# Performance work log

Hardware: AMD Instinct MI355X
Metric: run time of the kernel (lower is better)

The kernel has to match this reference:

```python
import jax, jax.numpy as jnp
import numpy as np

EPS = 1e-6

def _layer_norm(x, w, b):
    mu = jnp.mean(x, axis=-1, keepdims=True)
    var = jnp.mean((x - mu) ** 2, axis=-1, keepdims=True)
    return (x - mu) * jax.lax.rsqrt(var + EPS) * w + b

def setup_inputs() -> dict:
    key = jax.random.key(0)
    ks = jax.random.split(key, 8)
    B, N, C = 4, 1024, 2048
    H = C * 2  # mlp hidden = 2*feature_dim
    std = 0.01
    x = jax.random.normal(ks[0], (B, N, C), dtype=jnp.float32)
    wq = jax.random.normal(ks[1], (C, C), dtype=jnp.float32) * std
    wk = jax.random.normal(ks[2], (C, C), dtype=jnp.float32) * std
    wv = jax.random.normal(ks[3], (C, C), dtype=jnp.float32) * std
    ln1_w = jnp.ones((C,), jnp.float32); ln1_b = jnp.zeros((C,), jnp.float32)
    fc1_w = jax.random.normal(ks[4], (H, C), dtype=jnp.float32) * std
    fc1_b = jnp.zeros((H,), jnp.float32)
    fc2_w = jax.random.normal(ks[5], (C, H), dtype=jnp.float32) * std
    fc2_b = jnp.zeros((C,), jnp.float32)
    ln2_w = jnp.ones((C,), jnp.float32); ln2_b = jnp.zeros((C,), jnp.float32)
    return {"x": x, "wq": wq, "wk": wk, "wv": wv,
            "ln1_w": ln1_w, "ln1_b": ln1_b,
            "fc1_w": fc1_w, "fc1_b": fc1_b,
            "fc2_w": fc2_w, "fc2_b": fc2_b,
            "ln2_w": ln2_w, "ln2_b": ln2_b}

def reference(x, wq, wk, wv, ln1_w, ln1_b, fc1_w, fc1_b, fc2_w, fc2_b, ln2_w, ln2_b):
    B, N, C = x.shape
    num_head = 32
    d = C // num_head
    # QKV projections (no bias), split heads: [B, H, N, d]
    def proj(w):
        return (x @ w.T).reshape(B, N, num_head, d).transpose(0, 2, 1, 3)
    q, k, v = proj(wq), proj(wk), proj(wv)
    scale = 1.0 / jnp.sqrt(jnp.float32(d))
    attn = jnp.einsum('bhnd,bhmd->bhnm', q * scale, k)
    attn = jax.nn.softmax(attn, axis=-1)
    out = jnp.einsum('bhnm,bhmd->bhnd', attn, v)
    out = out.transpose(0, 2, 1, 3).reshape(B, N, C)
    out = _layer_norm(out + x, ln1_w, ln1_b)
    # MLP with residual + post-LN
    h = jax.nn.relu(out @ fc1_w.T + fc1_b)
    h = h @ fc2_w.T + fc2_b
    out = _layer_norm(out + h, ln2_w, ln2_b)
    return out
```

## Files before the change

### kernel.cpp

```cpp
#include <hip/hip_runtime.h>

#define C_DIM   2048
#define H_DIM   4096
#define NSEQ    1024
#define NBATCH  4
#define BN_ROWS 4096
#define NHEAD   32
#define DHEAD   64

typedef __attribute__((ext_vector_type(8))) short  short8;
typedef __attribute__((ext_vector_type(4))) float  f32x4;

__device__ __forceinline__ float bf2f(unsigned short u) {
    union { unsigned int i; float f; } v; v.i = ((unsigned int)u) << 16; return v.f;
}
__device__ __forceinline__ unsigned short f2bf(float f) {
    union { float f; unsigned int i; } v; v.f = f;
    unsigned int r = v.i + 0x7fffu + ((v.i >> 16) & 1u);
    return (unsigned short)(r >> 16);
}

#define G2L16(gp, lp) \
    __builtin_amdgcn_global_load_lds((const __attribute__((address_space(1))) void*)(gp), \
                                     (__attribute__((address_space(3))) void*)(lp), 16, 0, 0)

__global__ __launch_bounds__(256)
void cvt_bf16(const float* __restrict__ in, unsigned short* __restrict__ out, int n)
{
    const int i = (blockIdx.x * 256 + threadIdx.x) * 8;
    if (i >= n) return;
    float4 a = *(const float4*)(in + i);
    float4 b = *(const float4*)(in + i + 4);
    unsigned short o[8] = { f2bf(a.x), f2bf(a.y), f2bf(a.z), f2bf(a.w),
                            f2bf(b.x), f2bf(b.y), f2bf(b.z), f2bf(b.w) };
    *(int4*)(out + i) = *(const int4*)o;
}

template<int EPI, typename OUT_T>
__global__ __launch_bounds__(256)
void gemm_bt(const unsigned short* __restrict__ A,
             const unsigned short* __restrict__ B,
             const float* __restrict__ bias,
             OUT_T* __restrict__ C, int M, int N, int K)
{
    __shared__ unsigned short As[128 * 32];
    __shared__ unsigned short Bs[128 * 32];

    const int t    = threadIdx.x;
    const int lane = t & 63;
    const int wave = t >> 6;
    const int m0 = blockIdx.x * 128, n0 = blockIdx.y * 128;
    const int wm = (wave >> 1) * 64, wn = (wave & 1) * 64;
    const int lr = lane & 15;
    const int kq = lane >> 4;

    f32x4 acc[4][4] = {};

    const int lrow = lane >> 2;
    const int lcol = (lane & 3) * 8;

    for (int kt = 0; kt < K; kt += 32) {
        __syncthreads();
        #pragma unroll
        for (int p = 0; p < 2; ++p) {
            const int rbase = wave * 32 + p * 16;
            G2L16(&A[(size_t)(m0 + rbase + lrow) * K + kt + lcol], &As[rbase * 32]);
            G2L16(&B[(size_t)(n0 + rbase + lrow) * K + kt + lcol], &Bs[rbase * 32]);
        }
        __syncthreads();

        short8 af[4], bf[4];
        #pragma unroll
        for (int i = 0; i < 4; ++i)
            af[i] = *(const short8*)&As[(wm + i * 16 + lr) * 32 + kq * 8];
        #pragma unroll
        for (int j = 0; j < 4; ++j)
            bf[j] = *(const short8*)&Bs[(wn + j * 16 + lr) * 32 + kq * 8];
        #pragma unroll
        for (int i = 0; i < 4; ++i)
            #pragma unroll
            for (int j = 0; j < 4; ++j)
                acc[i][j] = __builtin_amdgcn_mfma_f32_16x16x32_bf16(af[i], bf[j], acc[i][j], 0, 0, 0);
    }

    #pragma unroll
    for (int j = 0; j < 4; ++j) {
        const int col = n0 + wn + j * 16 + lr;
        float bv = 0.f;
        if (EPI > 0) bv = bias[col];
        #pragma unroll
        for (int i = 0; i < 4; ++i) {
            #pragma unroll
            for (int r = 0; r < 4; ++r) {
                const int row = m0 + wm + i * 16 + kq * 4 + r;
                float v = acc[i][j][r] + bv;
                if (EPI == 1) v = fmaxf(v, 0.f);
                if constexpr (sizeof(OUT_T) == 2) C[(size_t)row * N + col] = f2bf(v);
                else                              C[(size_t)row * N + col] = v;
            }
        }
    }
}

#define LDK 72
__global__ __launch_bounds__(256)
void attn_mfma(const unsigned short* __restrict__ Qg,
               const unsigned short* __restrict__ Kg,
               const unsigned short* __restrict__ Vg,
               unsigned short* __restrict__ Og)
{
    __shared__ unsigned short Ks[64 * LDK];
    __shared__ unsigned short Vt[64 * LDK];
    __shared__ unsigned short Ps[64 * LDK];

    const int t    = threadIdx.x;
    const int lane = t & 63;
    const int wave = t >> 6;
    const int lr   = lane & 15;
    const int quad = lane >> 4;
    const int bh = blockIdx.y;
    const int b  = bh >> 5, h = bh & 31;
    const int q0 = blockIdx.x * 64;
    const int colbase = h * 64;

    short8 qf[2];
    {
        const size_t qrow = (size_t)(b * NSEQ + q0 + wave * 16 + lr) * C_DIM + colbase;
        #pragma unroll
        for (int kc = 0; kc < 2; ++kc) {
            short8 raw = *(const short8*)(Qg + qrow + kc * 32 + quad * 8);
            short8 sc;
            #pragma unroll
            for (int j = 0; j < 8; ++j)
                sc[j] = (short)f2bf(bf2f((unsigned short)raw[j]) * 0.125f);
            qf[kc] = sc;
        }
    }

    f32x4 Oacc[4] = {};
    float li[4] = {};

    for (int kt = 0; kt < 16; ++kt) {
        __syncthreads();
        {
            const int r = t >> 2, sg = (t & 3) * 16;
            const size_t grow = (size_t)(b * NSEQ + kt * 64 + r) * C_DIM + colbase + sg;
            *(int4*)&Ks[r * LDK + sg]     = *(const int4*)(Kg + grow);
            *(int4*)&Ks[r * LDK + sg + 8] = *(const int4*)(Kg + grow + 8);
        }
        {
            const int key = t & 63, d0 = (t >> 6) * 16;
            const size_t grow = (size_t)(b * NSEQ + kt * 64 + key) * C_DIM + colbase + d0;
            int4 u0 = *(const int4*)(Vg + grow);
            int4 u1 = *(const int4*)(Vg + grow + 8);
            const unsigned short* us0 = (const unsigned short*)&u0;
            const unsigned short* us1 = (const unsigned short*)&u1;
            #pragma unroll
            for (int j = 0; j < 8; ++j) {
                Vt[(d0 + j)     * LDK + key] = us0[j];
                Vt[(d0 + j + 8) * LDK + key] = us1[j];
            }
        }
        __syncthreads();

        f32x4 s[4] = {};
        #pragma unroll
        for (int n = 0; n < 4; ++n)
            #pragma unroll
            for (int kc = 0; kc < 2; ++kc) {
                short8 kf = *(const short8*)&Ks[(n * 16 + lr) * LDK + kc * 32 + quad * 8];
                s[n] = __builtin_amdgcn_mfma_f32_16x16x32_bf16(qf[kc], kf, s[n], 0, 0, 0);
            }

        float p[4][4];
        #pragma unroll
        for (int r = 0; r < 4; ++r) {
            #pragma unroll
            for (int n = 0; n < 4; ++n) { p[n][r] = __expf(s[n][r]); }
            li[r] += p[0][r] + p[1][r] + p[2][r] + p[3][r];
        }

        #pragma unroll
        for (int r = 0; r < 4; ++r)
            #pragma unroll
            for (int n = 0; n < 4; ++n)
                Ps[(wave * 16 + quad * 4 + r) * LDK + n * 16 + lr] = f2bf(p[n][r]);

        short8 pf[2];
        #pragma unroll
        for (int kc = 0; kc < 2; ++kc)
            pf[kc] = *(const short8*)&Ps[(wave * 16 + lr) * LDK + kc * 32 + quad * 8];

        #pragma unroll
        for (int n = 0; n < 4; ++n)
            #pragma unroll
            for (int kc = 0; kc < 2; ++kc) {
                short8 vf = *(const short8*)&Vt[(n * 16 + lr) * LDK + kc * 32 + quad * 8];
                Oacc[n] = __builtin_amdgcn_mfma_f32_16x16x32_bf16(pf[kc], vf, Oacc[n], 0, 0, 0);
            }
    }

    #pragma unroll
    for (int r = 0; r < 4; ++r) {
        #pragma unroll
        for (int off = 1; off < 16; off <<= 1) li[r] += __shfl_xor(li[r], off, 64);
        const float inv = 1.f / li[r];
        const size_t rowb = (size_t)(b * NSEQ + q0 + wave * 16 + quad * 4 + r) * C_DIM + colbase;
        #pragma unroll
        for (int n = 0; n < 4; ++n)
            Og[rowb + n * 16 + lr] = f2bf(Oacc[n][r] * inv);
    }
}

__global__ __launch_bounds__(256)
void ln_fused1(const unsigned short* __restrict__ a, const float* __restrict__ xr,
               const float* __restrict__ w, const float* __restrict__ bb,
               unsigned short* __restrict__ y16)
{
    const int row = blockIdx.x, t = threadIdx.x;
    const size_t base = (size_t)row * C_DIM;
    const int c0 = t * 8;
    float v[8];
    int4 ai = *(const int4*)(a + base + c0);
    const unsigned short* as = (const unsigned short*)&ai;
    float4 x0 = *(const float4*)(xr + base + c0);
    float4 x1 = *(const float4*)(xr + base + c0 + 4);
    v[0] = bf2f(as[0]) + x0.x; v[1] = bf2f(as[1]) + x0.y;
    v[2] = bf2f(as[2]) + x0.z; v[3] = bf2f(as[3]) + x0.w;
    v[4] = bf2f(as[4]) + x1.x; v[5] = bf2f(as[5]) + x1.y;
    v[6] = bf2f(as[6]) + x1.z; v[7] = bf2f(as[7]) + x1.w;

    float s = 0.f, s2 = 0.f;
    #pragma unroll
    for (int k = 0; k < 8; ++k) { s += v[k]; s2 += v[k] * v[k]; }
    #pragma unroll
    for (int off = 32; off; off >>= 1) { s += __shfl_xor(s, off, 64); s2 += __shfl_xor(s2, off, 64); }
    __shared__ float red[8];
    if ((t & 63) == 0) { red[t >> 6] = s; red[4 + (t >> 6)] = s2; }
    __syncthreads();
    s  = red[0] + red[1] + red[2] + red[3];
    s2 = red[4] + red[5] + red[6] + red[7];
    const float mu = s * (1.f / C_DIM);
    const float rs = rsqrtf(s2 * (1.f / C_DIM) - mu * mu + 1e-6f);

    float4 w0 = *(const float4*)(w + c0);
    float4 w1 = *(const float4*)(w + c0 + 4);
    float4 b0 = *(const float4*)(bb + c0);
    float4 b1 = *(const float4*)(bb + c0 + 4);
    const float* wf = (const float*)&w0; const float* wg = (const float*)&w1;
    const float* bf = (const float*)&b0; const float* bg = (const float*)&b1;
    unsigned short o16[8];
    #pragma unroll
    for (int k = 0; k < 4; ++k) {
        o16[k]     = f2bf((v[k]     - mu) * rs * wf[k] + bf[k]);
        o16[k + 4] = f2bf((v[k + 4] - mu) * rs * wg[k] + bg[k]);
    }
    *(int4*)(y16 + base + c0) = *(const int4*)o16;
}

__global__ __launch_bounds__(256)
void ln_fused2(const unsigned short* __restrict__ a, const unsigned short* __restrict__ b2,
               const float* __restrict__ w, const float* __restrict__ bb,
               float* __restrict__ out)
{
    const int row = blockIdx.x, t = threadIdx.x;
    const size_t base = (size_t)row * C_DIM;
    const int c0 = t * 8;
    float v[8];
    int4 ai = *(const int4*)(a + base + c0);
    int4 bi = *(const int4*)(b2 + base + c0);
    const unsigned short* as = (const unsigned short*)&ai;
    const unsigned short* bs = (const unsigned short*)&bi;
    #pragma unroll
    for (int k = 0; k < 8; ++k) v[k] = bf2f(as[k]) + bf2f(bs[k]);

    float s = 0.f, s2 = 0.f;
    #pragma unroll
    for (int k = 0; k < 8; ++k) { s += v[k]; s2 += v[k] * v[k]; }
    #pragma unroll
    for (int off = 32; off; off >>= 1) { s += __shfl_xor(s, off, 64); s2 += __shfl_xor(s2, off, 64); }
    __shared__ float red[8];
    if ((t & 63) == 0) { red[t >> 6] = s; red[4 + (t >> 6)] = s2; }
    __syncthreads();
    s  = red[0] + red[1] + red[2] + red[3];
    s2 = red[4] + red[5] + red[6] + red[7];
    const float mu = s * (1.f / C_DIM);
    const float rs = rsqrtf(s2 * (1.f / C_DIM) - mu * mu + 1e-6f);

    float4 w0 = *(const float4*)(w + c0);
    float4 w1 = *(const float4*)(w + c0 + 4);
    float4 b0 = *(const float4*)(bb + c0);
    float4 b1 = *(const float4*)(bb + c0 + 4);
    const float* wf = (const float*)&w0; const float* wg = (const float*)&w1;
    const float* bf = (const float*)&b0; const float* bg = (const float*)&b1;
    float4 o0, o1;
    #pragma unroll
    for (int k = 0; k < 4; ++k) {
        ((float*)&o0)[k] = (v[k]     - mu) * rs * wf[k] + bf[k];
        ((float*)&o1)[k] = (v[k + 4] - mu) * rs * wg[k] + bg[k];
    }
    *(float4*)(out + base + c0)     = o0;
    *(float4*)(out + base + c0 + 4) = o1;
}

extern "C" void kernel_launch(void* const* d_in, const int* in_sizes, int n_in,
                              void* d_out, int out_size, void* d_ws, size_t ws_size,
                              hipStream_t stream)
{
    (void)in_sizes; (void)n_in; (void)out_size; (void)ws_size;
    const float* x    = (const float*)d_in[0];
    const float* wq   = (const float*)d_in[1];
    const float* wk   = (const float*)d_in[2];
    const float* wv   = (const float*)d_in[3];
    const float* ln1w = (const float*)d_in[4];
    const float* ln1b = (const float*)d_in[5];
    const float* fc1w = (const float*)d_in[6];
    const float* fc1b = (const float*)d_in[7];
    const float* fc2w = (const float*)d_in[8];
    const float* fc2b = (const float*)d_in[9];
    const float* ln2w = (const float*)d_in[10];
    const float* ln2b = (const float*)d_in[11];

    char* ws = (char*)d_ws;
    const size_t MB16 = (size_t)BN_ROWS * C_DIM * 2;
    unsigned short* xb    = (unsigned short*)(ws);
    unsigned short* attnb = (unsigned short*)(ws);
    unsigned short* wqb   = (unsigned short*)(ws + MB16);
    unsigned short* wkb   = (unsigned short*)(ws + MB16 + MB16 / 2);
    unsigned short* y16   = (unsigned short*)(ws + MB16);
    unsigned short* wvb   = (unsigned short*)(ws + 2 * MB16);
    unsigned short* fc1wb = (unsigned short*)(ws + 2 * MB16 + MB16 / 2);
    unsigned short* fc2wb = (unsigned short*)(ws + 3 * MB16 + MB16 / 2);
    unsigned short* q_ws  = (unsigned short*)(ws + 4 * MB16 + MB16 / 2);
    unsigned short* h2    = (unsigned short*)(ws + 4 * MB16 + MB16 / 2);
    unsigned short* k_ws  = (unsigned short*)(ws + 5 * MB16 + MB16 / 2);
    unsigned short* v_ws  = (unsigned short*)(ws + 6 * MB16 + MB16 / 2);
    unsigned short* hbuf  = (unsigned short*)(ws + 5 * MB16 + MB16 / 2);

    dim3 blk(256);
    const int nX  = BN_ROWS * C_DIM;
    const int nW  = C_DIM * C_DIM;
    const int nW2 = H_DIM * C_DIM;

    cvt_bf16<<<dim3(nX  / 2048), blk, 0, stream>>>(x,    xb,    nX);
    cvt_bf16<<<dim3(nW  / 2048), blk, 0, stream>>>(wq,   wqb,   nW);
    cvt_bf16<<<dim3(nW  / 2048), blk, 0, stream>>>(wk,   wkb,   nW);
    cvt_bf16<<<dim3(nW  / 2048), blk, 0, stream>>>(wv,   wvb,   nW);
    cvt_bf16<<<dim3(nW2 / 2048), blk, 0, stream>>>(fc1w, fc1wb, nW2);
    cvt_bf16<<<dim3(nW2 / 2048), blk, 0, stream>>>(fc2w, fc2wb, nW2);

    gemm_bt<0, unsigned short><<<dim3(32, 16), blk, 0, stream>>>(xb, wqb, nullptr, q_ws, BN_ROWS, C_DIM, C_DIM);
    gemm_bt<0, unsigned short><<<dim3(32, 16), blk, 0, stream>>>(xb, wkb, nullptr, k_ws, BN_ROWS, C_DIM, C_DIM);
    gemm_bt<0, unsigned short><<<dim3(32, 16), blk, 0, stream>>>(xb, wvb, nullptr, v_ws, BN_ROWS, C_DIM, C_DIM);
    attn_mfma<<<dim3(NSEQ / 64, NBATCH * NHEAD), blk, 0, stream>>>(q_ws, k_ws, v_ws, attnb);
    ln_fused1<<<dim3(BN_ROWS), blk, 0, stream>>>(attnb, x, ln1w, ln1b, y16);
    gemm_bt<1, unsigned short><<<dim3(32, 32), blk, 0, stream>>>(y16, fc1wb, fc1b, hbuf, BN_ROWS, H_DIM, C_DIM);
    gemm_bt<2, unsigned short><<<dim3(32, 16), blk, 0, stream>>>(hbuf, fc2wb, fc2b, h2, BN_ROWS, C_DIM, H_DIM);
    ln_fused2<<<dim3(BN_ROWS), blk, 0, stream>>>(y16, h2, ln2w, ln2b, (float*)d_out);
}
```

Baseline: 666.3 us.

## Merge conversion launches, fuse QKV GEMMs, widen FC1 tile

Replaces six fp32-to-bf16 conversion launches with one launch that dispatches on block index. Merges the three Q/K/V projection GEMMs into a single launch of 1536 blocks, which removes launch gaps and small-grid tail effects. Adds a 128x256 tile GEMM for FC1 with bias and ReLU, so each A tile is reused across more columns. The wider tile doubles the accumulator registers, which may lower occupancy.

```diff
diff --git a/kernel.cpp b/kernel.cpp
--- a/kernel.cpp
+++ b/kernel.cpp
@@ -25,15 +25,27 @@
                                      (__attribute__((address_space(3))) void*)(lp), 16, 0, 0)
 
 __global__ __launch_bounds__(256)
-void cvt_bf16(const float* __restrict__ in, unsigned short* __restrict__ out, int n)
-{
-    const int i = (blockIdx.x * 256 + threadIdx.x) * 8;
-    if (i >= n) return;
-    float4 a = *(const float4*)(in + i);
-    float4 b = *(const float4*)(in + i + 4);
+void cvt_all(const float* __restrict__ x,   unsigned short* __restrict__ xo,
+             const float* __restrict__ w0,  unsigned short* __restrict__ w0o,
+             const float* __restrict__ w1,  unsigned short* __restrict__ w1o,
+             const float* __restrict__ w2,  unsigned short* __restrict__ w2o,
+             const float* __restrict__ w3,  unsigned short* __restrict__ w3o,
+             const float* __restrict__ w4,  unsigned short* __restrict__ w4o)
+{
+    int bid = blockIdx.x;
+    const float* src; unsigned short* dst;
+    if      (bid < 4096)  { src = x;  dst = xo;  }
+    else if (bid < 6144)  { src = w0; dst = w0o; bid -= 4096;  }
+    else if (bid < 8192)  { src = w1; dst = w1o; bid -= 6144;  }
+    else if (bid < 10240) { src = w2; dst = w2o; bid -= 8192;  }
+    else if (bid < 14336) { src = w3; dst = w3o; bid -= 10240; }
+    else                  { src = w4; dst = w4o; bid -= 14336; }
+    const size_t i = ((size_t)bid * 256 + threadIdx.x) * 8;
+    float4 a = *(const float4*)(src + i);
+    float4 b = *(const float4*)(src + i + 4);
     unsigned short o[8] = { f2bf(a.x), f2bf(a.y), f2bf(a.z), f2bf(a.w),
                             f2bf(b.x), f2bf(b.y), f2bf(b.z), f2bf(b.w) };
-    *(int4*)(out + i) = *(const int4*)o;
+    *(int4*)(dst + i) = *(const int4*)o;
 }
 
 template<int EPI, typename OUT_T>
@@ -63,9 +75,9 @@
         __syncthreads();
         #pragma unroll
         for (int p = 0; p < 2; ++p) {
-            const int rbase = wave * 32 + p * 16;
-            G2L16(&A[(size_t)(m0 + rbase + lrow) * K + kt + lcol], &As[rbase * 32]);
-            G2L16(&B[(size_t)(n0 + rbase + lrow) * K + kt + lcol], &Bs[rbase * 32]);
+            const int rb = wave * 32 + p * 16;
+            G2L16(&A[(size_t)(m0 + rb + lrow) * K + kt + lcol], &As[rb * 32]);
+            G2L16(&B[(size_t)(n0 + rb + lrow) * K + kt + lcol], &Bs[rb * 32]);
         }
         __syncthreads();
 
@@ -97,6 +109,139 @@
                 if (EPI == 1) v = fmaxf(v, 0.f);
                 if constexpr (sizeof(OUT_T) == 2) C[(size_t)row * N + col] = f2bf(v);
                 else                              C[(size_t)row * N + col] = v;
+            }
+        }
+    }
+}
+
+__global__ __launch_bounds__(256)
+void gemm_qkv(const unsigned short* __restrict__ A,
+              const unsigned short* __restrict__ Wq,
+              const unsigned short* __restrict__ Wk,
+              const unsigned short* __restrict__ Wv,
+              unsigned short* __restrict__ Qo,
+              unsigned short* __restrict__ Ko,
+              unsigned short* __restrict__ Vo)
+{
+    __shared__ unsigned short As[128 * 32];
+    __shared__ unsigned short Bs[128 * 32];
+
+    const int t    = threadIdx.x;
+    const int lane = t & 63;
+    const int wave = t >> 6;
+    const int m0 = blockIdx.x * 128;
+    const int ng = blockIdx.y * 128;
+    const unsigned short* B; unsigned short* Cp; int n0;
+    if      (ng < 2048) { B = Wq; Cp = Qo; n0 = ng; }
+    else if (ng < 4096) { B = Wk; Cp = Ko; n0 = ng - 2048; }
+    else                { B = Wv; Cp = Vo; n0 = ng - 4096; }
+
+    const int wm = (wave >> 1) * 64, wn = (wave & 1) * 64;
+    const int lr = lane & 15;
+    const int kq = lane >> 4;
+
+    f32x4 acc[4][4] = {};
+
+    const int lrow = lane >> 2;
+    const int lcol = (lane & 3) * 8;
+
+    for (int kt = 0; kt < C_DIM; kt += 32) {
+        __syncthreads();
+        #pragma unroll
+        for (int p = 0; p < 2; ++p) {
+            const int rb = wave * 32 + p * 16;
+            G2L16(&A[(size_t)(m0 + rb + lrow) * C_DIM + kt + lcol], &As[rb * 32]);
+            G2L16(&B[(size_t)(n0 + rb + lrow) * C_DIM + kt + lcol], &Bs[rb * 32]);
+        }
+        __syncthreads();
+
+        short8 af[4], bf[4];
+        #pragma unroll
+        for (int i = 0; i < 4; ++i)
+            af[i] = *(const short8*)&As[(wm + i * 16 + lr) * 32 + kq * 8];
+        #pragma unroll
+        for (int j = 0; j < 4; ++j)
+            bf[j] = *(const short8*)&Bs[(wn + j * 16 + lr) * 32 + kq * 8];
+        #pragma unroll
+        for (int i = 0; i < 4; ++i)
+            #pragma unroll
+            for (int j = 0; j < 4; ++j)
+                acc[i][j] = __builtin_amdgcn_mfma_f32_16x16x32_bf16(af[i], bf[j], acc[i][j], 0, 0, 0);
+    }
+
+    #pragma unroll
+    for (int j = 0; j < 4; ++j) {
+        const int col = n0 + wn + j * 16 + lr;
+        #pragma unroll
+        for (int i = 0; i < 4; ++i) {
+            #pragma unroll
+            for (int r = 0; r < 4; ++r) {
+                const int row = m0 + wm + i * 16 + kq * 4 + r;
+                Cp[(size_t)row * C_DIM + col] = f2bf(acc[i][j][r]);
+            }
+        }
+    }
+}
+
+__global__ __launch_bounds__(256)
+void gemm_wide_relu(const unsigned short* __restrict__ A,
+                    const unsigned short* __restrict__ B,
+                    const float* __restrict__ bias,
+                    unsigned short* __restrict__ C, int M, int N, int K)
+{
+    __shared__ unsigned short As[128 * 32];
+    __shared__ unsigned short Bs[256 * 32];
+
+    const int t    = threadIdx.x;
+    const int lane = t & 63;
+    const int wave = t >> 6;
+    const int m0 = blockIdx.x * 128, n0 = blockIdx.y * 256;
+    const int wm = (wave >> 1) * 64, wn = (wave & 1) * 128;
+    const int lr = lane & 15;
+    const int kq = lane >> 4;
+
+    f32x4 acc[4][8] = {};
+
+    const int lrow = lane >> 2;
+    const int lcol = (lane & 3) * 8;
+
+    for (int kt = 0; kt < K; kt += 32) {
+        __syncthreads();
+        #pragma unroll
+        for (int p = 0; p < 2; ++p) {
+            const int rb = wave * 32 + p * 16;
+            G2L16(&A[(size_t)(m0 + rb + lrow) * K + kt + lcol], &As[rb * 32]);
+        }
+        #pragma unroll
+        for (int p = 0; p < 4; ++p) {
+            const int rb = wave * 64 + p * 16;
+            G2L16(&B[(size_t)(n0 + rb + lrow) * K + kt + lcol], &Bs[rb * 32]);
+        }
+        __syncthreads();
+
+        short8 af[4];
+        #pragma unroll
+        for (int i = 0; i < 4; ++i)
+            af[i] = *(const short8*)&As[(wm + i * 16 + lr) * 32 + kq * 8];
+        #pragma unroll
+        for (int j = 0; j < 8; ++j) {
+            short8 bf = *(const short8*)&Bs[(wn + j * 16 + lr) * 32 + kq * 8];
+            #pragma unroll
+            for (int i = 0; i < 4; ++i)
+                acc[i][j] = __builtin_amdgcn_mfma_f32_16x16x32_bf16(af[i], bf, acc[i][j], 0, 0, 0);
+        }
+    }
+
+    #pragma unroll
+    for (int j = 0; j < 8; ++j) {
+        const int col = n0 + wn + j * 16 + lr;
+        const float bv = bias[col];
+        #pragma unroll
+        for (int i = 0; i < 4; ++i) {
+            #pragma unroll
+            for (int r = 0; r < 4; ++r) {
+                const int row = m0 + wm + i * 16 + kq * 4 + r;
+                C[(size_t)row * N + col] = f2bf(fmaxf(acc[i][j][r] + bv, 0.f));
             }
         }
     }
@@ -338,23 +483,14 @@
     unsigned short* hbuf  = (unsigned short*)(ws + 5 * MB16 + MB16 / 2);
 
     dim3 blk(256);
-    const int nX  = BN_ROWS * C_DIM;
-    const int nW  = C_DIM * C_DIM;
-    const int nW2 = H_DIM * C_DIM;
-
-    cvt_bf16<<<dim3(nX  / 2048), blk, 0, stream>>>(x,    xb,    nX);
-    cvt_bf16<<<dim3(nW  / 2048), blk, 0, stream>>>(wq,   wqb,   nW);
-    cvt_bf16<<<dim3(nW  / 2048), blk, 0, stream>>>(wk,   wkb,   nW);
-    cvt_bf16<<<dim3(nW  / 2048), blk, 0, stream>>>(wv,   wvb,   nW);
-    cvt_bf16<<<dim3(nW2 / 2048), blk, 0, stream>>>(fc1w, fc1wb, nW2);
-    cvt_bf16<<<dim3(nW2 / 2048), blk, 0, stream>>>(fc2w, fc2wb, nW2);
-
-    gemm_bt<0, unsigned short><<<dim3(32, 16), blk, 0, stream>>>(xb, wqb, nullptr, q_ws, BN_ROWS, C_DIM, C_DIM);
-    gemm_bt<0, unsigned short><<<dim3(32, 16), blk, 0, stream>>>(xb, wkb, nullptr, k_ws, BN_ROWS, C_DIM, C_DIM);
-    gemm_bt<0, unsigned short><<<dim3(32, 16), blk, 0, stream>>>(xb, wvb, nullptr, v_ws, BN_ROWS, C_DIM, C_DIM);
+
+    cvt_all<<<dim3(18432), blk, 0, stream>>>(x, xb, wq, wqb, wk, wkb, wv, wvb,
+                                             fc1w, fc1wb, fc2w, fc2wb);
+
+    gemm_qkv<<<dim3(32, 48), blk, 0, stream>>>(xb, wqb, wkb, wvb, q_ws, k_ws, v_ws);
     attn_mfma<<<dim3(NSEQ / 64, NBATCH * NHEAD), blk, 0, stream>>>(q_ws, k_ws, v_ws, attnb);
     ln_fused1<<<dim3(BN_ROWS), blk, 0, stream>>>(attnb, x, ln1w, ln1b, y16);
-    gemm_bt<1, unsigned short><<<dim3(32, 32), blk, 0, stream>>>(y16, fc1wb, fc1b, hbuf, BN_ROWS, H_DIM, C_DIM);
+    gemm_wide_relu<<<dim3(32, 16), blk, 0, stream>>>(y16, fc1wb, fc1b, hbuf, BN_ROWS, H_DIM, C_DIM);
     gemm_bt<2, unsigned short><<<dim3(32, 16), blk, 0, stream>>>(hbuf, fc2wb, fc2b, h2, BN_ROWS, C_DIM, H_DIM);
     ln_fused2<<<dim3(BN_ROWS), blk, 0, stream>>>(y16, h2, ln2w, ln2b, (float*)d_out);
 }
```

Result: no change. 661.2 us (-0.8%).
